# Optimization experiments

Hardware: AMD Instinct MI355X
Metric: run time of the kernel (lower is better)

Reference implementation:

```python
import jax, jax.numpy as jnp
import numpy as np

N_VAR, N_CSTR, E, D = 100_000, 50_000, 1_000_000, 64
BN_EPS = 1e-5


def setup_inputs() -> dict:
    key = jax.random.key(0)
    ks = jax.random.split(key, 12)
    s = 0.05
    return {
        "var_feats": jax.random.normal(ks[0], (N_VAR, D), jnp.float32),
        "cstr_feats": jax.random.normal(ks[1], (N_CSTR, D), jnp.float32),
        "edge_src": jax.random.randint(ks[2], (E,), 0, N_CSTR),  # cstr indices
        "edge_dst": jax.random.randint(ks[3], (E,), 0, N_VAR),   # var indices
        "edge_attr": jax.random.normal(ks[4], (E,), jnp.float32),
        # BatchNorm affine params
        "node_bn_gamma": jnp.ones((D,), jnp.float32),
        "node_bn_beta": jnp.zeros((D,), jnp.float32),
        "cstr_bn_gamma": jnp.ones((D,), jnp.float32),
        "cstr_bn_beta": jnp.zeros((D,), jnp.float32),
        # node_gnn = GraphConv(in=(cstr_dim, node_dim), out=node_dim, aggr='mean')
        "node_rel_w": s * jax.random.normal(ks[5], (D, D), jnp.float32),
        "node_rel_b": s * jax.random.normal(ks[6], (D,), jnp.float32),
        "node_root_w": s * jax.random.normal(ks[7], (D, D), jnp.float32),
        # cstr_gnn = GraphConv(in=(node_dim, cstr_dim), out=cstr_dim, aggr='mean')
        "cstr_rel_w": s * jax.random.normal(ks[8], (D, D), jnp.float32),
        "cstr_rel_b": s * jax.random.normal(ks[9], (D,), jnp.float32),
        "cstr_root_w": s * jax.random.normal(ks[10], (D, D), jnp.float32),
    }


def _batch_norm(x, gamma, beta):
    # training-mode BatchNorm1d over the node axis (biased variance)
    m = jnp.mean(x, axis=0)
    v = jnp.var(x, axis=0)
    return (x - m) * jax.lax.rsqrt(v + BN_EPS) * gamma + beta


def _graph_conv(x_src, x_dst, src, dst, ew, w_rel, b_rel, w_root):
    # message: edge_weight * x_src[src], scatter-mean onto destinations
    msg = x_src[src] * ew                                   # [E, D]
    n_dst = x_dst.shape[0]
    ssum = jax.ops.segment_sum(msg, dst, num_segments=n_dst)          # [n_dst, D]
    cnt = jax.ops.segment_sum(jnp.ones((src.shape[0],), x_dst.dtype), dst,
                              num_segments=n_dst)                     # [n_dst]
    agg = ssum / jnp.maximum(cnt, 1.0)[:, None]
    return agg @ w_rel.T + b_rel + x_dst @ w_root.T


def reference(var_feats, cstr_feats, edge_src, edge_dst, edge_attr,
              node_bn_gamma, node_bn_beta, cstr_bn_gamma, cstr_bn_beta,
              node_rel_w, node_rel_b, node_root_w,
              cstr_rel_w, cstr_rel_b, cstr_root_w):
    x_node = _batch_norm(var_feats, node_bn_gamma, node_bn_beta)
    x_cstr = _batch_norm(cstr_feats, cstr_bn_gamma, cstr_bn_beta)
    ew = edge_attr[:, None]                                  # [E, 1]
    # node_gnn: source = cstr, dst = node (edge_index as given)
    x_node_ = _graph_conv(x_cstr, x_node, edge_src, edge_dst, ew,
                          node_rel_w, node_rel_b, node_root_w)
    # cstr_gnn: flipped edge_index -> source = node, dst = cstr
    x_cstr_ = _graph_conv(x_node, x_cstr, edge_dst, edge_src, ew,
                          cstr_rel_w, cstr_rel_b, cstr_root_w)
    x_node_ = jax.nn.relu(x_node_ + x_node)  # residual=True
    x_cstr_ = jax.nn.relu(x_cstr_ + x_cstr)
    return x_node_, x_cstr_
```

## Files before the change

### kernel.cpp

```cpp
#include <hip/hip_runtime.h>

#define N_VAR   100000
#define N_CSTR  50000
#define NEDGE   1000000
#define DIM     64

#define NBK_N 782
#define NBK_C 391
#define NBK_T 1173
#define NCHUNK 245

#define OFF_STATS  0
#define OFF_BHIST  256
#define OFF_AB     1536
#define OFF_GBN    1792
#define OFF_GBC    2592
#define OFF_GCN    3008
#define OFF_GCC    3808
#define OFF_OFF_N  4224
#define OFF_OFF_C  104228
#define OFF_XCB    154232
#define OFF_XNB    1754232
#define OFF_ENT_N  4954232
#define OFF_ENT_C  6954232
#define WS_ZERO_N  1536

typedef __attribute__((ext_vector_type(8))) short bf16x8;
typedef __attribute__((ext_vector_type(4))) float f32x4;

__global__ __launch_bounds__(256) void bn_stats_k(const float* __restrict__ x, int n,
                                                  float* __restrict__ stats) {
  int c = threadIdx.x & 63;
  int rg = threadIdx.x >> 6;
  float s = 0.f, q = 0.f;
  for (int r = blockIdx.x * 4 + rg; r < n; r += gridDim.x * 4) {
    float v = x[r * DIM + c];
    s += v;
    q += v * v;
  }
  __shared__ float sb[256], qb[256];
  sb[threadIdx.x] = s;
  qb[threadIdx.x] = q;
  __syncthreads();
  if (rg == 0) {
    s = sb[c] + sb[c + 64] + sb[c + 128] + sb[c + 192];
    q = qb[c] + qb[c + 64] + qb[c + 128] + qb[c + 192];
    atomicAdd(&stats[c], s);
    atomicAdd(&stats[64 + c], q);
  }
}

__global__ void bn_finalize_k(const float* __restrict__ stats,
                              const float* __restrict__ gn, const float* __restrict__ bn,
                              const float* __restrict__ gc, const float* __restrict__ bc,
                              float* __restrict__ ab) {
  int t = threadIdx.x;
  int c = t & 63;
  bool isC = t >= 64;
  const float* st = stats + (isC ? 128 : 0);
  float n = isC ? (float)N_CSTR : (float)N_VAR;
  float mean = st[c] / n;
  float var = st[64 + c] / n - mean * mean;
  float g = isC ? gc[c] : gn[c];
  float be = isC ? bc[c] : bn[c];
  float a = g * rsqrtf(var + 1e-5f);
  float b = be - mean * a;
  float* o = ab + (isC ? 128 : 0);
  o[c] = a;
  o[64 + c] = b;
}

__device__ __forceinline__ unsigned short f2bf(float f) {
  unsigned u = __float_as_uint(f);
  return (unsigned short)((u + 0x7FFFu + ((u >> 16) & 1u)) >> 16);
}

__global__ __launch_bounds__(256) void cvt_k(const float4* __restrict__ src4,
                                             const float* __restrict__ ab,
                                             ushort4* __restrict__ dst, int n4) {
  int i4 = blockIdx.x * 256 + threadIdx.x;
  if (i4 >= n4) return;
  float4 v = src4[i4];
  int c0 = (i4 << 2) & 63;
  ushort4 o;
  o.x = f2bf(fmaf(v.x, ab[c0 + 0], ab[64 + c0 + 0]));
  o.y = f2bf(fmaf(v.y, ab[c0 + 1], ab[64 + c0 + 1]));
  o.z = f2bf(fmaf(v.z, ab[c0 + 2], ab[64 + c0 + 2]));
  o.w = f2bf(fmaf(v.w, ab[c0 + 3], ab[64 + c0 + 3]));
  dst[i4] = o;
}

__global__ __launch_bounds__(256) void bhist_k(const int4* __restrict__ es4,
                                               const int4* __restrict__ ed4,
                                               int* __restrict__ ws) {
  __shared__ int h[1280];
  for (int i = threadIdx.x; i < 1280; i += 256) h[i] = 0;
  __syncthreads();
  int stride = gridDim.x * 256;
  for (int i4 = blockIdx.x * 256 + threadIdx.x; i4 < NEDGE / 4; i4 += stride) {
    int4 d = ed4[i4];
    int4 s = es4[i4];
    atomicAdd(&h[d.x >> 7], 1);
    atomicAdd(&h[d.y >> 7], 1);
    atomicAdd(&h[d.z >> 7], 1);
    atomicAdd(&h[d.w >> 7], 1);
    atomicAdd(&h[NBK_N + (s.x >> 7)], 1);
    atomicAdd(&h[NBK_N + (s.y >> 7)], 1);
    atomicAdd(&h[NBK_N + (s.z >> 7)], 1);
    atomicAdd(&h[NBK_N + (s.w >> 7)], 1);
  }
  __syncthreads();
  int* gh = ws + OFF_BHIST;
  for (int i = threadIdx.x; i < NBK_T; i += 256)
    if (h[i]) atomicAdd(&gh[i], h[i]);
}

__global__ __launch_bounds__(256) void bscan_k(int* __restrict__ ws) {
  __shared__ int sb[256];
  int t = threadIdx.x;
#pragma unroll
  for (int seg = 0; seg < 2; ++seg) {
    int nbk = seg ? NBK_C : NBK_N;
    const int* h = ws + OFF_BHIST + (seg ? NBK_N : 0);
    int* gb = ws + (seg ? OFF_GBC : OFF_GBN);
    int* gc = ws + (seg ? OFF_GCC : OFF_GCN);
    int base = t * 4;
    int c[4];
    int s0 = 0;
#pragma unroll
    for (int j = 0; j < 4; ++j) {
      c[j] = (base + j < nbk) ? h[base + j] : 0;
      s0 += c[j];
    }
    sb[t] = s0;
    __syncthreads();
    for (int d = 1; d < 256; d <<= 1) {
      int v = (t >= d) ? sb[t - d] : 0;
      __syncthreads();
      sb[t] += v;
      __syncthreads();
    }
    int ex = sb[t] - s0;
#pragma unroll
    for (int j = 0; j < 4; ++j) {
      if (base + j < nbk) {
        gb[base + j] = ex;
        gc[base + j] = ex;
      }
      ex += c[j];
    }
    if (t == 255) gb[nbk] = sb[255];
    __syncthreads();
  }
  if (t == 0) {
    ws[OFF_OFF_N + N_VAR] = NEDGE;
    ws[OFF_OFF_C + N_CSTR] = NEDGE;
  }
}

__global__ __launch_bounds__(256) void passA_k(const int4* __restrict__ es4,
                                               const int4* __restrict__ ed4,
                                               const float4* __restrict__ ea4,
                                               int* __restrict__ ws) {
  __shared__ int cntL[1024];
  __shared__ int runoffL[1024];
  __shared__ int gblL[1024];
  __shared__ int2 dataL[4096];
  __shared__ unsigned short bidL[4096];
  __shared__ int sbL[256];
  int side = (blockIdx.x >= NCHUNK);
  int chunk = side ? blockIdx.x - NCHUNK : blockIdx.x;
  int nbk = side ? NBK_C : NBK_N;
  int* gcur = ws + (side ? OFF_GCC : OFF_GCN);
  int2* ent = (int2*)(ws + (side ? OFF_ENT_C : OFF_ENT_N));
  int t = threadIdx.x;
  for (int i = t; i < 1024; i += 256) cntL[i] = 0;
  __syncthreads();
  int e0 = chunk * 4096;
  int base4 = chunk * 1024 + t * 4;
  int pk[16];
  int2 pay[16];
#pragma unroll
  for (int j = 0; j < 4; ++j) {
    int i4 = base4 + j;
    if (i4 < NEDGE / 4) {
      int4 sv = es4[i4];
      int4 dv = ed4[i4];
      float4 wv = ea4[i4];
      int ss[4] = {sv.x, sv.y, sv.z, sv.w};
      int dd[4] = {dv.x, dv.y, dv.z, dv.w};
      float ww[4] = {wv.x, wv.y, wv.z, wv.w};
#pragma unroll
      for (int k = 0; k < 4; ++k) {
        int s = ss[k], d = dd[k];
        int b = side ? (s >> 7) : (d >> 7);
        int pl = side ? (d | ((s & 127) << 17)) : (s | ((d & 127) << 17));
        int rank = atomicAdd(&cntL[b], 1);
        pk[j * 4 + k] = b * 4096 + rank;
        pay[j * 4 + k] = make_int2(pl, __float_as_int(ww[k]));
      }
    } else {
#pragma unroll
      for (int k = 0; k < 4; ++k) pk[j * 4 + k] = -1;
    }
  }
  __syncthreads();
  int base = t * 4;
  int c[4];
  int s0 = 0;
#pragma unroll
  for (int j = 0; j < 4; ++j) {
    c[j] = cntL[base + j];
    s0 += c[j];
  }
  sbL[t] = s0;
  __syncthreads();
  for (int d = 1; d < 256; d <<= 1) {
    int v = (t >= d) ? sbL[t - d] : 0;
    __syncthreads();
    sbL[t] += v;
    __syncthreads();
  }
  int ex = sbL[t] - s0;
#pragma unroll
  for (int j = 0; j < 4; ++j) {
    runoffL[base + j] = ex;
    ex += c[j];
  }
  __syncthreads();
  for (int b = t; b < nbk; b += 256) {
    int cc = cntL[b];
    gblL[b] = cc ? atomicAdd(&gcur[b], cc) : 0;
  }
  __syncthreads();
#pragma unroll
  for (int j = 0; j < 16; ++j) {
    if (pk[j] >= 0) {
      int b = pk[j] >> 12;
      int slot = runoffL[b] + (pk[j] & 4095);
      dataL[slot] = pay[j];
      bidL[slot] = (unsigned short)b;
    }
  }
  __syncthreads();
  int chunkN = min(4096, NEDGE - e0);
  for (int i = t; i < chunkN; i += 256) {
    int b = bidL[i];
    ent[gblL[b] + (i - runoffL[b])] = dataL[i];
  }
}

__global__ __launch_bounds__(256) void sort_k(int* __restrict__ ws) {
  __shared__ int2 data[4096];
  __shared__ int hcnt[128], hrank[128];
  __shared__ int sb[128];
  int x = blockIdx.x;
  int side = (x >= NBK_N);
  int bk = side ? x - NBK_N : x;
  const int* gbase = ws + (side ? OFF_GBC : OFF_GBN);
  int2* ent = (int2*)(ws + (side ? OFF_ENT_C : OFF_ENT_N));
  int* off = ws + (side ? OFF_OFF_C : OFF_OFF_N);
  int n = side ? N_CSTR : N_VAR;
  int t = threadIdx.x;
  int beg = gbase[bk], end = gbase[bk + 1];
  int cnt = end - beg;
  if (t < 128) hcnt[t] = 0;
  __syncthreads();
  for (int i = t; i < cnt; i += 256) {
    int2 e = ent[beg + i];
    data[i] = e;
    atomicAdd(&hcnt[(e.x >> 17) & 127], 1);
  }
  __syncthreads();
  if (t < 128) sb[t] = hcnt[t];
  __syncthreads();
  for (int d = 1; d < 128; d <<= 1) {
    int v = 0;
    if (t < 128 && t >= d) v = sb[t - d];
    __syncthreads();
    if (t < 128) sb[t] += v;
    __syncthreads();
  }
  if (t < 128) {
    int ex = sb[t] - hcnt[t];
    hrank[t] = ex;
    int r = bk * 128 + t;
    if (r < n) off[r] = beg + ex;
  }
  __syncthreads();
  for (int i = t; i < cnt; i += 256) {
    int2 e = data[i];
    int dl = (e.x >> 17) & 127;
    int pos = atomicAdd(&hrank[dl], 1);
    ent[beg + pos] = make_int2(e.x & 0x1FFFF, e.y);
  }
}

__global__ __launch_bounds__(256) void gather_k(
    const unsigned short* __restrict__ tab, const int2* __restrict__ ent,
    const int* __restrict__ off, float* __restrict__ agg, int n) {
  int lane = threadIdx.x & 63;
  int r = __builtin_amdgcn_readfirstlane((blockIdx.x * blockDim.x + threadIdx.x) >> 6);
  if (r >= n) return;
  int beg = off[r], end = off[r + 1];
  float acc0 = 0.f, acc1 = 0.f;
  int e = beg;
#define BF(hv) __uint_as_float(((unsigned)(hv)) << 16)
  if (e < end && (e & 1)) {
    int2 p = ent[e];
    acc0 = fmaf(BF(tab[p.x * DIM + lane]), __int_as_float(p.y), acc0);
    ++e;
  }
  for (; e + 8 <= end; e += 8) {
    int4 p0 = *reinterpret_cast<const int4*>(&ent[e]);
    int4 p1 = *reinterpret_cast<const int4*>(&ent[e + 2]);
    int4 p2 = *reinterpret_cast<const int4*>(&ent[e + 4]);
    int4 p3 = *reinterpret_cast<const int4*>(&ent[e + 6]);
    float v0 = BF(tab[p0.x * DIM + lane]);
    float v1 = BF(tab[p0.z * DIM + lane]);
    float v2 = BF(tab[p1.x * DIM + lane]);
    float v3 = BF(tab[p1.z * DIM + lane]);
    float v4 = BF(tab[p2.x * DIM + lane]);
    float v5 = BF(tab[p2.z * DIM + lane]);
    float v6 = BF(tab[p3.x * DIM + lane]);
    float v7 = BF(tab[p3.z * DIM + lane]);
    acc0 = fmaf(v0, __int_as_float(p0.y), acc0);
    acc1 = fmaf(v1, __int_as_float(p0.w), acc1);
    acc0 = fmaf(v2, __int_as_float(p1.y), acc0);
    acc1 = fmaf(v3, __int_as_float(p1.w), acc1);
    acc0 = fmaf(v4, __int_as_float(p2.y), acc0);
    acc1 = fmaf(v5, __int_as_float(p2.w), acc1);
    acc0 = fmaf(v6, __int_as_float(p3.y), acc0);
    acc1 = fmaf(v7, __int_as_float(p3.w), acc1);
  }
  for (; e + 2 <= end; e += 2) {
    int4 p = *reinterpret_cast<const int4*>(&ent[e]);
    acc0 = fmaf(BF(tab[p.x * DIM + lane]), __int_as_float(p.y), acc0);
    acc1 = fmaf(BF(tab[p.z * DIM + lane]), __int_as_float(p.w), acc1);
  }
  if (e < end) {
    int2 p = ent[e];
    acc0 = fmaf(BF(tab[p.x * DIM + lane]), __int_as_float(p.y), acc0);
  }
#undef BF
  agg[(long)r * DIM + lane] = (acc0 + acc1) / fmaxf((float)(end - beg), 1.f);
}

__global__ __launch_bounds__(256) void out_mfma_k(
    const float* __restrict__ raw, const float* __restrict__ ab,
    const float* __restrict__ w_rel, const float* __restrict__ b_rel,
    const float* __restrict__ w_root, float* __restrict__ io, int n) {
  int t = threadIdx.x;
  int lane = t & 63, wv = t >> 6;
  int quad = lane >> 4, l16 = lane & 15;

  bf16x8 bfrag[4][4];
#pragma unroll
  for (int nt = 0; nt < 4; ++nt) {
    int c = nt * 16 + l16;
#pragma unroll
    for (int kc = 0; kc < 4; ++kc) {
      int bk = kc * 32 + quad * 8;
      const float* wsrc = (bk < 64) ? (w_rel + c * 64 + bk) : (w_root + c * 64 + bk - 64);
      bf16x8 f;
#pragma unroll
      for (int j = 0; j < 8; ++j) f[j] = (short)f2bf(wsrc[j]);
      bfrag[nt][kc] = f;
    }
  }
  float av0[8], bv0[8], av1[8], bv1[8];
#pragma unroll
  for (int j = 0; j < 8; ++j) {
    av0[j] = ab[quad * 8 + j];
    bv0[j] = ab[64 + quad * 8 + j];
    av1[j] = ab[32 + quad * 8 + j];
    bv1[j] = ab[96 + quad * 8 + j];
  }

  int tiles = n >> 4;
  for (int tile = blockIdx.x * 4 + wv; tile < tiles; tile += gridDim.x * 4) {
    int r0 = tile << 4;
    const float* aggr = io + (long)(r0 + l16) * DIM;
    const float* rawr = raw + (long)(r0 + l16) * DIM;
    bf16x8 a0, a1, a2, a3;
#pragma unroll
    for (int j = 0; j < 8; ++j) {
      a0[j] = (short)f2bf(aggr[quad * 8 + j]);
      a1[j] = (short)f2bf(aggr[32 + quad * 8 + j]);
      a2[j] = (short)f2bf(fmaf(rawr[quad * 8 + j], av0[j], bv0[j]));
      a3[j] = (short)f2bf(fmaf(rawr[32 + quad * 8 + j], av1[j], bv1[j]));
    }
    f32x4 acc[4];
#pragma unroll
    for (int nt = 0; nt < 4; ++nt) {
      acc[nt] = (f32x4){0.f, 0.f, 0.f, 0.f};
      acc[nt] = __builtin_amdgcn_mfma_f32_16x16x32_bf16(a0, bfrag[nt][0], acc[nt], 0, 0, 0);
      acc[nt] = __builtin_amdgcn_mfma_f32_16x16x32_bf16(a1, bfrag[nt][1], acc[nt], 0, 0, 0);
      acc[nt] = __builtin_amdgcn_mfma_f32_16x16x32_bf16(a2, bfrag[nt][2], acc[nt], 0, 0, 0);
      acc[nt] = __builtin_amdgcn_mfma_f32_16x16x32_bf16(a3, bfrag[nt][3], acc[nt], 0, 0, 0);
    }
#pragma unroll
    for (int nt = 0; nt < 4; ++nt) {
      int c = nt * 16 + l16;
      float aC = ab[c], bC = ab[64 + c], brC = b_rel[c];
#pragma unroll
      for (int reg = 0; reg < 4; ++reg) {
        int r = r0 + quad * 4 + reg;
        float xv = fmaf(raw[(long)r * DIM + c], aC, bC);
        io[(long)r * DIM + c] = fmaxf(acc[nt][reg] + brC + xv, 0.f);
      }
    }
  }
}

extern "C" void kernel_launch(void* const* d_in, const int* in_sizes, int n_in,
                              void* d_out, int out_size, void* d_ws, size_t ws_size,
                              hipStream_t stream) {
  const float* vf = (const float*)d_in[0];
  const float* cf = (const float*)d_in[1];
  const int* es = (const int*)d_in[2];
  const int* ed = (const int*)d_in[3];
  const float* ea = (const float*)d_in[4];
  const float* gn = (const float*)d_in[5];
  const float* bn = (const float*)d_in[6];
  const float* gc = (const float*)d_in[7];
  const float* bc = (const float*)d_in[8];
  const float* n_rel_w = (const float*)d_in[9];
  const float* n_rel_b = (const float*)d_in[10];
  const float* n_root_w = (const float*)d_in[11];
  const float* c_rel_w = (const float*)d_in[12];
  const float* c_rel_b = (const float*)d_in[13];
  const float* c_root_w = (const float*)d_in[14];
  float* out = (float*)d_out;
  int* wsi = (int*)d_ws;
  float* wsf = (float*)d_ws;

  float* stats = wsf + OFF_STATS;
  float* ab = wsf + OFF_AB;
  ushort4* xcb = (ushort4*)(wsi + OFF_XCB);
  ushort4* xnb = (ushort4*)(wsi + OFF_XNB);
  const unsigned short* xcb_s = (const unsigned short*)(wsi + OFF_XCB);
  const unsigned short* xnb_s = (const unsigned short*)(wsi + OFF_XNB);
  const int2* ent_n = (const int2*)(wsi + OFF_ENT_N);
  const int2* ent_c = (const int2*)(wsi + OFF_ENT_C);

  float* agg_node = out;
  float* agg_cstr = out + (long)N_VAR * DIM;

  hipMemsetAsync(d_ws, 0, (size_t)WS_ZERO_N * sizeof(int), stream);

  bn_stats_k<<<512, 256, 0, stream>>>(vf, N_VAR, stats);
  bn_stats_k<<<512, 256, 0, stream>>>(cf, N_CSTR, stats + 128);
  bn_finalize_k<<<1, 128, 0, stream>>>(stats, gn, bn, gc, bc, ab);

  cvt_k<<<(N_CSTR * DIM / 4 + 255) / 256, 256, 0, stream>>>((const float4*)cf, ab + 128,
                                                            xcb, N_CSTR * DIM / 4);
  cvt_k<<<(N_VAR * DIM / 4 + 255) / 256, 256, 0, stream>>>((const float4*)vf, ab,
                                                           xnb, N_VAR * DIM / 4);

  bhist_k<<<128, 256, 0, stream>>>((const int4*)es, (const int4*)ed, wsi);
  bscan_k<<<1, 256, 0, stream>>>(wsi);
  passA_k<<<2 * NCHUNK, 256, 0, stream>>>((const int4*)es, (const int4*)ed,
                                          (const float4*)ea, wsi);
  sort_k<<<NBK_T, 256, 0, stream>>>(wsi);

  gather_k<<<(N_VAR + 3) / 4, 256, 0, stream>>>(xcb_s, ent_n, wsi + OFF_OFF_N,
                                                agg_node, N_VAR);
  gather_k<<<(N_CSTR + 3) / 4, 256, 0, stream>>>(xnb_s, ent_c, wsi + OFF_OFF_C,
                                                 agg_cstr, N_CSTR);

  out_mfma_k<<<640, 256, 0, stream>>>(vf, ab, n_rel_w, n_rel_b, n_root_w,
                                      agg_node, N_VAR);
  out_mfma_k<<<320, 256, 0, stream>>>(cf, ab + 128, c_rel_w, c_rel_b, c_root_w,
                                      agg_cstr, N_CSTR);
}
```

Before: 333.8 us.

## Fuse bucket sort with per-row gather into one kernel using LDS-sorted edges

Merges the per-bucket counting sort and the two CSR gather kernels into a single kernel. Each block sorts its bucket's edges into shared memory and then has its four waves gather-accumulate the 128 destination rows directly from LDS. This removes the write-back of sorted edges, the offsets array and two kernel launches. The cost is lower gather parallelism: 1173 blocks with four waves each, serial per-row loops, and the LDS footprint limiting occupancy.

```diff
diff --git a/kernel.cpp b/kernel.cpp
--- a/kernel.cpp
+++ b/kernel.cpp
@@ -17,8 +17,6 @@
 #define OFF_GBC    2592
 #define OFF_GCN    3008
 #define OFF_GCC    3808
-#define OFF_OFF_N  4224
-#define OFF_OFF_C  104228
 #define OFF_XCB    154232
 #define OFF_XNB    1754232
 #define OFF_ENT_N  4954232
@@ -152,10 +150,6 @@
     if (t == 255) gb[nbk] = sb[255];
     __syncthreads();
   }
-  if (t == 0) {
-    ws[OFF_OFF_N + N_VAR] = NEDGE;
-    ws[OFF_OFF_C + N_CSTR] = NEDGE;
-  }
 }
 
 __global__ __launch_bounds__(256) void passA_k(const int4* __restrict__ es4,
@@ -250,16 +244,19 @@
   }
 }
 
-__global__ __launch_bounds__(256) void sort_k(int* __restrict__ ws) {
-  __shared__ int2 data[4096];
-  __shared__ int hcnt[128], hrank[128];
+__global__ __launch_bounds__(256) void sortgather_k(int* __restrict__ ws,
+                                                    float* __restrict__ outbase) {
+  __shared__ int2 sorted[4096];
+  __shared__ int hcnt[128], hoff[128], hrank[128];
   __shared__ int sb[128];
   int x = blockIdx.x;
   int side = (x >= NBK_N);
   int bk = side ? x - NBK_N : x;
   const int* gbase = ws + (side ? OFF_GBC : OFF_GBN);
-  int2* ent = (int2*)(ws + (side ? OFF_ENT_C : OFF_ENT_N));
-  int* off = ws + (side ? OFF_OFF_C : OFF_OFF_N);
+  const int2* ent = (const int2*)(ws + (side ? OFF_ENT_C : OFF_ENT_N));
+  const unsigned short* tab =
+      (const unsigned short*)(ws + (side ? OFF_XNB : OFF_XCB));
+  float* agg = side ? outbase + (long)N_VAR * DIM : outbase;
   int n = side ? N_CSTR : N_VAR;
   int t = threadIdx.x;
   int beg = gbase[bk], end = gbase[bk + 1];
@@ -268,7 +265,6 @@
   __syncthreads();
   for (int i = t; i < cnt; i += 256) {
     int2 e = ent[beg + i];
-    data[i] = e;
     atomicAdd(&hcnt[(e.x >> 17) & 127], 1);
   }
   __syncthreads();
@@ -283,67 +279,46 @@
   }
   if (t < 128) {
     int ex = sb[t] - hcnt[t];
+    hoff[t] = ex;
     hrank[t] = ex;
-    int r = bk * 128 + t;
-    if (r < n) off[r] = beg + ex;
   }
   __syncthreads();
   for (int i = t; i < cnt; i += 256) {
-    int2 e = data[i];
+    int2 e = ent[beg + i];
     int dl = (e.x >> 17) & 127;
     int pos = atomicAdd(&hrank[dl], 1);
-    ent[beg + pos] = make_int2(e.x & 0x1FFFF, e.y);
-  }
-}
-
-__global__ __launch_bounds__(256) void gather_k(
-    const unsigned short* __restrict__ tab, const int2* __restrict__ ent,
-    const int* __restrict__ off, float* __restrict__ agg, int n) {
-  int lane = threadIdx.x & 63;
-  int r = __builtin_amdgcn_readfirstlane((blockIdx.x * blockDim.x + threadIdx.x) >> 6);
-  if (r >= n) return;
-  int beg = off[r], end = off[r + 1];
-  float acc0 = 0.f, acc1 = 0.f;
-  int e = beg;
+    sorted[pos] = make_int2(e.x & 0x1FFFF, e.y);
+  }
+  __syncthreads();
+  int lane = t & 63, wv = t >> 6;
 #define BF(hv) __uint_as_float(((unsigned)(hv)) << 16)
-  if (e < end && (e & 1)) {
-    int2 p = ent[e];
-    acc0 = fmaf(BF(tab[p.x * DIM + lane]), __int_as_float(p.y), acc0);
-    ++e;
-  }
-  for (; e + 8 <= end; e += 8) {
-    int4 p0 = *reinterpret_cast<const int4*>(&ent[e]);
-    int4 p1 = *reinterpret_cast<const int4*>(&ent[e + 2]);
-    int4 p2 = *reinterpret_cast<const int4*>(&ent[e + 4]);
-    int4 p3 = *reinterpret_cast<const int4*>(&ent[e + 6]);
-    float v0 = BF(tab[p0.x * DIM + lane]);
-    float v1 = BF(tab[p0.z * DIM + lane]);
-    float v2 = BF(tab[p1.x * DIM + lane]);
-    float v3 = BF(tab[p1.z * DIM + lane]);
-    float v4 = BF(tab[p2.x * DIM + lane]);
-    float v5 = BF(tab[p2.z * DIM + lane]);
-    float v6 = BF(tab[p3.x * DIM + lane]);
-    float v7 = BF(tab[p3.z * DIM + lane]);
-    acc0 = fmaf(v0, __int_as_float(p0.y), acc0);
-    acc1 = fmaf(v1, __int_as_float(p0.w), acc1);
-    acc0 = fmaf(v2, __int_as_float(p1.y), acc0);
-    acc1 = fmaf(v3, __int_as_float(p1.w), acc1);
-    acc0 = fmaf(v4, __int_as_float(p2.y), acc0);
-    acc1 = fmaf(v5, __int_as_float(p2.w), acc1);
-    acc0 = fmaf(v6, __int_as_float(p3.y), acc0);
-    acc1 = fmaf(v7, __int_as_float(p3.w), acc1);
-  }
-  for (; e + 2 <= end; e += 2) {
-    int4 p = *reinterpret_cast<const int4*>(&ent[e]);
-    acc0 = fmaf(BF(tab[p.x * DIM + lane]), __int_as_float(p.y), acc0);
-    acc1 = fmaf(BF(tab[p.z * DIM + lane]), __int_as_float(p.w), acc1);
-  }
-  if (e < end) {
-    int2 p = ent[e];
-    acc0 = fmaf(BF(tab[p.x * DIM + lane]), __int_as_float(p.y), acc0);
+  for (int j = wv; j < 128; j += 4) {
+    int r = bk * 128 + j;
+    if (r >= n) break;
+    int rb = hoff[j], rc = hcnt[j];
+    float acc0 = 0.f, acc1 = 0.f;
+    int i = 0;
+    for (; i + 4 <= rc; i += 4) {
+      int2 e0 = sorted[rb + i];
+      int2 e1 = sorted[rb + i + 1];
+      int2 e2 = sorted[rb + i + 2];
+      int2 e3 = sorted[rb + i + 3];
+      float v0 = BF(tab[e0.x * DIM + lane]);
+      float v1 = BF(tab[e1.x * DIM + lane]);
+      float v2 = BF(tab[e2.x * DIM + lane]);
+      float v3 = BF(tab[e3.x * DIM + lane]);
+      acc0 = fmaf(v0, __int_as_float(e0.y), acc0);
+      acc1 = fmaf(v1, __int_as_float(e1.y), acc1);
+      acc0 = fmaf(v2, __int_as_float(e2.y), acc0);
+      acc1 = fmaf(v3, __int_as_float(e3.y), acc1);
+    }
+    for (; i < rc; ++i) {
+      int2 e0 = sorted[rb + i];
+      acc0 = fmaf(BF(tab[e0.x * DIM + lane]), __int_as_float(e0.y), acc0);
+    }
+    agg[(long)r * DIM + lane] = (acc0 + acc1) / fmaxf((float)rc, 1.f);
   }
 #undef BF
-  agg[(long)r * DIM + lane] = (acc0 + acc1) / fmaxf((float)(end - beg), 1.f);
 }
 
 __global__ __launch_bounds__(256) void out_mfma_k(
@@ -439,10 +414,6 @@
   float* ab = wsf + OFF_AB;
   ushort4* xcb = (ushort4*)(wsi + OFF_XCB);
   ushort4* xnb = (ushort4*)(wsi + OFF_XNB);
-  const unsigned short* xcb_s = (const unsigned short*)(wsi + OFF_XCB);
-  const unsigned short* xnb_s = (const unsigned short*)(wsi + OFF_XNB);
-  const int2* ent_n = (const int2*)(wsi + OFF_ENT_N);
-  const int2* ent_c = (const int2*)(wsi + OFF_ENT_C);
 
   float* agg_node = out;
   float* agg_cstr = out + (long)N_VAR * DIM;
@@ -462,12 +433,7 @@
   bscan_k<<<1, 256, 0, stream>>>(wsi);
   passA_k<<<2 * NCHUNK, 256, 0, stream>>>((const int4*)es, (const int4*)ed,
                                           (const float4*)ea, wsi);
-  sort_k<<<NBK_T, 256, 0, stream>>>(wsi);
-
-  gather_k<<<(N_VAR + 3) / 4, 256, 0, stream>>>(xcb_s, ent_n, wsi + OFF_OFF_N,
-                                                agg_node, N_VAR);
-  gather_k<<<(N_CSTR + 3) / 4, 256, 0, stream>>>(xnb_s, ent_c, wsi + OFF_OFF_C,
-                                                 agg_cstr, N_CSTR);
+  sortgather_k<<<NBK_T, 256, 0, stream>>>(wsi, out);
 
   out_mfma_k<<<640, 256, 0, stream>>>(vf, ab, n_rel_w, n_rel_b, n_root_w,
                                       agg_node, N_VAR);
```

Measured after the change: 367.7 us. 1.1x slower.
